# Performance work log

Hardware: AMD Instinct MI355X
Metric: run time of the kernel (lower is better)

Reference implementation:

```python
import jax, jax.numpy as jnp
import numpy as np

N, E, DIM, HEADS = 40000, 640000, 128, 8
HD = DIM // HEADS  # per-head dim
NEG_SLOPE = 0.2


def setup_inputs() -> dict:
    key = jax.random.key(0)
    ks = jax.random.split(key, 10)
    s = 1.0 / np.sqrt(DIM)
    return {
        "x": jax.random.normal(ks[0], (N, DIM), dtype=jnp.float32),
        "edge_index": jax.random.randint(ks[1], (2, E), 0, N, dtype=jnp.int64),
        "W_src": jax.random.normal(ks[2], (DIM, DIM), dtype=jnp.float32) * s,
        "b_src": jnp.zeros((DIM,), dtype=jnp.float32),
        "W_dst": jax.random.normal(ks[3], (DIM, DIM), dtype=jnp.float32) * s,
        "b_dst": jnp.zeros((DIM,), dtype=jnp.float32),
        "att": jax.random.normal(ks[4], (HEADS, HD), dtype=jnp.float32) * (1.0 / np.sqrt(HD)),
        "bias_out": jnp.zeros((DIM,), dtype=jnp.float32),
        "ln_gamma": jnp.ones((DIM,), dtype=jnp.float32),
        "ln_beta": jnp.zeros((DIM,), dtype=jnp.float32),
    }


def reference(x, edge_index, W_src, b_src, W_dst, b_dst, att, bias_out, ln_gamma, ln_beta):
    n = x.shape[0]
    # PyG GATv2Conv default: add self loops
    loops = jnp.arange(n, dtype=edge_index.dtype)
    src = jnp.concatenate([edge_index[0], loops])  # message source j
    dst = jnp.concatenate([edge_index[1], loops])  # message target i

    xs = (x @ W_src + b_src).reshape(n, HEADS, HD)  # [N,H,C]
    xd = (x @ W_dst + b_dst).reshape(n, HEADS, HD)

    # per-edge GATv2 attention logits
    e = xs[src] + xd[dst]                                   # [Et,H,C]
    e = jnp.where(e >= 0, e, NEG_SLOPE * e)                 # LeakyReLU(0.2)
    logits = jnp.einsum('ehc,hc->eh', e, att)               # [Et,H]

    # segment softmax over incoming edges of each dst node
    m = jax.ops.segment_max(logits, dst, num_segments=n)    # [N,H]
    ex = jnp.exp(logits - m[dst])
    denom = jax.ops.segment_sum(ex, dst, num_segments=n)    # [N,H]
    alpha = ex / denom[dst]                                  # [Et,H]

    # weighted scatter-add of source features
    msg = xs[src] * alpha[:, :, None]                       # [Et,H,C]
    out = jax.ops.segment_sum(msg, dst, num_segments=n)     # [N,H,C]
    out = out.reshape(n, DIM) + bias_out

    # dropout is identity in eval mode; residual + LayerNorm + GELU
    h = out + x
    mu = jnp.mean(h, axis=-1, keepdims=True)
    var = jnp.var(h, axis=-1, keepdims=True)
    h = (h - mu) / jnp.sqrt(var + 1e-5) * ln_gamma + ln_beta
    return jax.nn.gelu(h, approximate=False)
```

## Files before the change

kernel.cpp:

```cpp
#include <hip/hip_runtime.h>

typedef unsigned int uint;
typedef unsigned short ushort;
typedef __attribute__((ext_vector_type(8))) short short8;
typedef __attribute__((ext_vector_type(4))) float f32x4;

__device__ __forceinline__ float b2f(ushort u) {
    return __uint_as_float(((uint)u) << 16);
}
__device__ __forceinline__ ushort f2b(float f) {
    uint u = __float_as_uint(f);
    u += 0x7FFFu + ((u >> 16) & 1u);
    return (ushort)(u >> 16);
}
__device__ __forceinline__ float fast_exp2(float v) {
    float r;
    asm volatile("v_exp_f32 %0, %1" : "=v"(r) : "v"(v));
    return r;
}

template<int CTRL>
__device__ __forceinline__ float dpp_add(float v) {
    int s = __float_as_int(v);
    int d = __builtin_amdgcn_update_dpp(s, s, CTRL, 0xF, 0xF, true);
    return v + __int_as_float(d);
}

#define LDW 136

__global__ __launch_bounds__(512) void gemm_kernel(
    const float* __restrict__ x,
    const float* __restrict__ Wsrc, const float* __restrict__ bsrc,
    const float* __restrict__ Wdst, const float* __restrict__ bdst,
    ushort* __restrict__ xs, float* __restrict__ xd,
    int n, int* __restrict__ deg)
{
    __shared__ ushort WtS[128 * LDW];
    __shared__ ushort WtD[128 * LDW];
    int t = threadIdx.x;
    int gid = blockIdx.x * 512 + t;
    if (gid < n) deg[gid] = 1;
    for (int i = t * 4; i < 128 * 128; i += 512 * 4) {
        int k = i >> 7, c = i & 127;
        float4 wS = *(const float4*)(Wsrc + i);
        float4 wD = *(const float4*)(Wdst + i);
        WtS[(c + 0) * LDW + k] = f2b(wS.x);
        WtS[(c + 1) * LDW + k] = f2b(wS.y);
        WtS[(c + 2) * LDW + k] = f2b(wS.z);
        WtS[(c + 3) * LDW + k] = f2b(wS.w);
        WtD[(c + 0) * LDW + k] = f2b(wD.x);
        WtD[(c + 1) * LDW + k] = f2b(wD.y);
        WtD[(c + 2) * LDW + k] = f2b(wD.z);
        WtD[(c + 3) * LDW + k] = f2b(wD.w);
    }
    __syncthreads();

    int wave = t >> 6, lane = t & 63;
    int r = lane & 15, q = lane >> 4;
    int row = blockIdx.x * 128 + wave * 16 + r;
    f32x4 accS[8], accD[8];
#pragma unroll
    for (int i = 0; i < 8; i++) { accS[i] = (f32x4)(0.f); accD[i] = (f32x4)(0.f); }

#pragma unroll
    for (int kk = 0; kk < 4; kk++) {
        float v[8];
#pragma unroll
        for (int j = 0; j < 8; j++) v[j] = 0.f;
        if (row < n) {
            const float4* src = (const float4*)(x + (size_t)row * 128 + kk * 32 + q * 8);
            float4 p0 = src[0], p1 = src[1];
            v[0] = p0.x; v[1] = p0.y; v[2] = p0.z; v[3] = p0.w;
            v[4] = p1.x; v[5] = p1.y; v[6] = p1.z; v[7] = p1.w;
        }
        short8 ah, al;
#pragma unroll
        for (int j = 0; j < 8; j++) {
            ushort h = f2b(v[j]);
            ah[j] = (short)h;
            al[j] = (short)f2b(v[j] - b2f(h));
        }
#pragma unroll
        for (int ct = 0; ct < 8; ct++) {
            int off = (ct * 16 + r) * LDW + kk * 32 + q * 8;
            short8 bS = *(const short8*)(WtS + off);
            short8 bD = *(const short8*)(WtD + off);
            accS[ct] = __builtin_amdgcn_mfma_f32_16x16x32_bf16(ah, bS, accS[ct], 0, 0, 0);
            accS[ct] = __builtin_amdgcn_mfma_f32_16x16x32_bf16(al, bS, accS[ct], 0, 0, 0);
            accD[ct] = __builtin_amdgcn_mfma_f32_16x16x32_bf16(ah, bD, accD[ct], 0, 0, 0);
            accD[ct] = __builtin_amdgcn_mfma_f32_16x16x32_bf16(al, bD, accD[ct], 0, 0, 0);
        }
    }
    int rbase = blockIdx.x * 128 + wave * 16 + q * 4;
#pragma unroll
    for (int ct = 0; ct < 8; ct++) {
        int col = ct * 16 + r;
        float bS = bsrc[col];
        float bD = bdst[col];
#pragma unroll
        for (int rg = 0; rg < 4; rg++) {
            int orow = rbase + rg;
            if (orow < n) {
                xs[(size_t)orow * 128 + col] = f2b(accS[ct][rg] + bS);
                xd[(size_t)orow * 128 + col] = accD[ct][rg] + bD;
            }
        }
    }
}

__global__ void count_kernel(const int* __restrict__ ei, int E,
                             int* __restrict__ deg) {
    __shared__ int f_s;
    if (threadIdx.x < 64) {
        int w = ei[2 * threadIdx.x + 1];
        unsigned long long nz = __ballot(w != 0);
        if (threadIdx.x == 0) f_s = (nz == 0ULL) ? 1 : 0;
    }
    __syncthreads();
    int f = f_s;
    int e = blockIdx.x * 256 + threadIdx.x;
    if (e < E) {
        int d = f ? ei[2 * E + 2 * e] : ei[E + e];
        atomicAdd(&deg[d], 1);
    }
}

__global__ __launch_bounds__(1024) void scan_blk(
    const int* __restrict__ deg, int* __restrict__ lpre,
    int* __restrict__ bsum, int n)
{
    __shared__ int ws[16];
    __shared__ int wp[16];
    int t = threadIdx.x, lane = t & 63, w = t >> 6;
    int g = blockIdx.x * 1024 + t;
    int v = (g < n) ? deg[g] : 0;
    int inc = v;
#pragma unroll
    for (int off = 1; off < 64; off <<= 1) {
        int sh = __shfl_up(inc, off);
        if (lane >= off) inc += sh;
    }
    if (lane == 63) ws[w] = inc;
    __syncthreads();
    if (t == 0) {
        int run = 0;
#pragma unroll
        for (int i = 0; i < 16; i++) { wp[i] = run; run += ws[i]; }
        bsum[blockIdx.x] = run;
    }
    __syncthreads();
    if (g < n) lpre[g] = wp[w] + inc - v;
}

__global__ __launch_bounds__(1024) void scan_fix(
    const int* __restrict__ lpre, const int* __restrict__ bsum,
    const int* __restrict__ deg, int* __restrict__ row_start,
    int* __restrict__ cursor, int n)
{
    __shared__ int boff_s;
    int t = threadIdx.x, b = blockIdx.x;
    if (t < 64) {
        int v = 0;
        for (int i = t; i < b; i += 64) v += bsum[i];
#pragma unroll
        for (int off = 32; off >= 1; off >>= 1) v += __shfl_xor(v, off);
        if (t == 0) boff_s = v;
    }
    __syncthreads();
    int g = b * 1024 + t;
    if (g < n) {
        int rs = lpre[g] + boff_s;
        row_start[g] = rs;
        cursor[g] = rs;
        if (g == n - 1) row_start[n] = rs + deg[g];
    }
}

__global__ void fill_kernel(const int* __restrict__ ei, int E, int n,
                            int* __restrict__ cursor, int* __restrict__ esrc) {
    __shared__ int f_s;
    if (threadIdx.x < 64) {
        int w = ei[2 * threadIdx.x + 1];
        unsigned long long nz = __ballot(w != 0);
        if (threadIdx.x == 0) f_s = (nz == 0ULL) ? 1 : 0;
    }
    __syncthreads();
    int f = f_s;
    int idx = blockIdx.x * 256 + threadIdx.x;
    if (idx < E) {
        int s = f ? ei[2 * idx]         : ei[idx];
        int d = f ? ei[2 * E + 2 * idx] : ei[E + idx];
        int pos = atomicAdd(&cursor[d], 1);
        esrc[pos] = s;
    } else if (idx < E + n) {
        int i = idx - E;
        int pos = atomicAdd(&cursor[i], 1);
        esrc[pos] = i;
    }
}

__global__ __launch_bounds__(64) void node_kernel(
    const ushort* __restrict__ xs, const float* __restrict__ xd,
    const float* __restrict__ x,  const float* __restrict__ att,
    const float* __restrict__ bias_out, const float* __restrict__ gamma,
    const float* __restrict__ beta,
    const int* __restrict__ row_start, const int* __restrict__ esrc,
    float* __restrict__ out, int n)
{
    int lane = threadIdx.x;
    int node = blockIdx.x;
    if (node >= n) return;
    int q = lane >> 4, r = lane & 15;
    int cb = r * 8;

    const float LOG2E = 1.44269504088896f;
    const float A = 0.6f * LOG2E, B = 0.4f * LOG2E;

    float xdc[8], atc[8];
    {
        const float4* xp = (const float4*)(xd + (size_t)node * 128 + cb);
        float4 p0 = xp[0], p1 = xp[1];
        xdc[0]=p0.x; xdc[1]=p0.y; xdc[2]=p0.z; xdc[3]=p0.w;
        xdc[4]=p1.x; xdc[5]=p1.y; xdc[6]=p1.z; xdc[7]=p1.w;
        const float4* ap = (const float4*)(att + cb);
        float4 a0 = ap[0], a1 = ap[1];
        atc[0]=a0.x; atc[1]=a0.y; atc[2]=a0.z; atc[3]=a0.w;
        atc[4]=a1.x; atc[5]=a1.y; atc[6]=a1.z; atc[7]=a1.w;
    }
    float KL = 0.f;
#pragma unroll
    for (int i = 0; i < 8; i++) KL = fmaf(atc[i], xdc[i], KL);
    KL *= A;

    int start = row_start[node], end = row_start[node + 1];
    int end1 = end - 1;
    float s = 0.f, acc[8];
#pragma unroll
    for (int i = 0; i < 8; i++) acc[i] = 0.f;

    uint cboff = (uint)(cb);
    int j0 = esrc[min(start + q, end1)];
    uint4 raw = *(const uint4*)(xs + (uint)j0 * 128u + cboff);

    for (int base = start; base < end; base += 4) {
        int jn = esrc[min(base + 4 + q, end1)];
        uint4 rawn = *(const uint4*)(xs + (uint)jn * 128u + cboff);

        float v[8];
        v[0] = __uint_as_float(raw.x << 16); v[1] = __uint_as_float(raw.x & 0xFFFF0000u);
        v[2] = __uint_as_float(raw.y << 16); v[3] = __uint_as_float(raw.y & 0xFFFF0000u);
        v[4] = __uint_as_float(raw.z << 16); v[5] = __uint_as_float(raw.z & 0xFFFF0000u);
        v[6] = __uint_as_float(raw.w << 16); v[7] = __uint_as_float(raw.w & 0xFFFF0000u);

        float dv = 0.f, da = 0.f;
#pragma unroll
        for (int i = 0; i < 8; i++) {
            dv = fmaf(atc[i], v[i], dv);
            da = fmaf(atc[i], fabsf(v[i] + xdc[i]), da);
        }
        float P = fmaf(A, dv, fmaf(B, da, KL));
        P = dpp_add<0xB1>(P);
        float p = fast_exp2(P);
        p = (base + q < end) ? p : 0.f;
        s += p;
#pragma unroll
        for (int i = 0; i < 8; i++) acc[i] = fmaf(p, v[i], acc[i]);

        raw = rawn;
    }

#pragma unroll
    for (int off = 16; off <= 32; off <<= 1) {
        s += __shfl_xor(s, off);
#pragma unroll
        for (int i = 0; i < 8; i++) acc[i] += __shfl_xor(acc[i], off);
    }

    float inv = 1.f / s;
    float o[8];
    {
        const float4* bp = (const float4*)(bias_out + cb);
        const float4* xp = (const float4*)(x + (size_t)node * 128 + cb);
        float4 b0 = bp[0], b1 = bp[1], x0 = xp[0], x1 = xp[1];
        o[0] = fmaf(acc[0], inv, b0.x + x0.x); o[1] = fmaf(acc[1], inv, b0.y + x0.y);
        o[2] = fmaf(acc[2], inv, b0.z + x0.z); o[3] = fmaf(acc[3], inv, b0.w + x0.w);
        o[4] = fmaf(acc[4], inv, b1.x + x1.x); o[5] = fmaf(acc[5], inv, b1.y + x1.y);
        o[6] = fmaf(acc[6], inv, b1.z + x1.z); o[7] = fmaf(acc[7], inv, b1.w + x1.w);
    }
    float ssum = 0.f, ssq = 0.f;
#pragma unroll
    for (int i = 0; i < 8; i++) {
        ssum += o[i];
        ssq  = fmaf(o[i], o[i], ssq);
    }
#pragma unroll
    for (int off = 1; off <= 8; off <<= 1) {
        ssum += __shfl_xor(ssum, off);
        ssq  += __shfl_xor(ssq, off);
    }
    float mean = ssum * (1.f / 128.f);
    float var  = ssq  * (1.f / 128.f) - mean * mean;
    float rstd = rsqrtf(var + 1e-5f);

    if (q == 0) {
        const float4* gp = (const float4*)(gamma + cb);
        const float4* ep = (const float4*)(beta + cb);
        float4 g0 = gp[0], g1 = gp[1], e0 = ep[0], e1 = ep[1];
        float gch[8] = {g0.x, g0.y, g0.z, g0.w, g1.x, g1.y, g1.z, g1.w};
        float ech[8] = {e0.x, e0.y, e0.z, e0.w, e1.x, e1.y, e1.z, e1.w};
        float res[8];
#pragma unroll
        for (int i = 0; i < 8; i++) {
            float g = (o[i] - mean) * rstd * gch[i] + ech[i];
            res[i] = 0.5f * g * (1.f + erff(g * 0.70710678118654752f));
        }
        float4* op = (float4*)(out + (size_t)node * 128 + cb);
        float4 r0, r1;
        r0.x = res[0]; r0.y = res[1]; r0.z = res[2]; r0.w = res[3];
        r1.x = res[4]; r1.y = res[5]; r1.z = res[6]; r1.w = res[7];
        op[0] = r0; op[1] = r1;
    }
}

extern "C" void kernel_launch(void* const* d_in, const int* in_sizes, int n_in,
                              void* d_out, int out_size, void* d_ws, size_t ws_size,
                              hipStream_t stream)
{
    const float* x    = (const float*)d_in[0];
    const int*   ei   = (const int*)d_in[1];
    const float* Wsrc = (const float*)d_in[2];
    const float* bsrc = (const float*)d_in[3];
    const float* Wdst = (const float*)d_in[4];
    const float* bdst = (const float*)d_in[5];
    const float* att  = (const float*)d_in[6];
    const float* bout = (const float*)d_in[7];
    const float* gam  = (const float*)d_in[8];
    const float* bet  = (const float*)d_in[9];
    float* out = (float*)d_out;

    int n = in_sizes[0] / 128;
    int E = in_sizes[1] / 2;

    char* p = (char*)d_ws;
    auto alloc = [&](size_t bytes) {
        char* q = p;
        p += (bytes + 255) & ~((size_t)255);
        return q;
    };
    ushort* xs        = (ushort*)alloc((size_t)n * 128 * 2);
    float*  xd        = (float*)alloc((size_t)n * 128 * 4);
    int*    deg       = (int*)alloc((size_t)n * 4);
    int*    row_start = (int*)alloc((size_t)(n + 1) * 4);
    int*    cursor    = (int*)alloc((size_t)n * 4);
    int*    esrc      = (int*)alloc((size_t)(E + n) * 4);
    int     nblk      = (n + 1023) / 1024;
    int*    lpre      = (int*)alloc((size_t)nblk * 1024 * 4);
    int*    bsum      = (int*)alloc((size_t)nblk * 4);

    hipLaunchKernelGGL(gemm_kernel, dim3((n + 127) / 128), dim3(512), 0, stream,
                       x, Wsrc, bsrc, Wdst, bdst, xs, xd, n, deg);
    hipLaunchKernelGGL(count_kernel, dim3((E + 255) / 256), dim3(256), 0, stream,
                       ei, E, deg);
    hipLaunchKernelGGL(scan_blk, dim3(nblk), dim3(1024), 0, stream,
                       deg, lpre, bsum, n);
    hipLaunchKernelGGL(scan_fix, dim3(nblk), dim3(1024), 0, stream,
                       lpre, bsum, deg, row_start, cursor, n);
    hipLaunchKernelGGL(fill_kernel, dim3((E + n + 255) / 256), dim3(256), 0, stream,
                       ei, E, n, cursor, esrc);
    hipLaunchKernelGGL(node_kernel, dim3(n), dim3(64), 0, stream,
                       xs, xd, x, att, bout, gam, bet, row_start, esrc, out, n);
}
```

Before: 221.4 us.

## Fuse CSR build into one persistent kernel with software grid barriers

Replaces the count, two-pass scan and fill kernels with a single 128-block persistent kernel that uses atomic-counter grid barriers between phases, and reads edge indices with vectorized uint4 loads. Degree init moves to a memset. The node kernel drops the min() clamp on esrc by padding esrc with 64 zeros, and gets a launch_bounds occupancy hint. This removes several kernel launches and their inter-kernel gaps, but the fused kernel runs on only 128 blocks, which may underuse the device for the atomic scatter phases. The spin barriers also rely on every block being resident at once.

```diff
diff --git a/kernel.cpp b/kernel.cpp
--- a/kernel.cpp
+++ b/kernel.cpp
@@ -32,14 +32,11 @@
     const float* __restrict__ x,
     const float* __restrict__ Wsrc, const float* __restrict__ bsrc,
     const float* __restrict__ Wdst, const float* __restrict__ bdst,
-    ushort* __restrict__ xs, float* __restrict__ xd,
-    int n, int* __restrict__ deg)
+    ushort* __restrict__ xs, float* __restrict__ xd, int n)
 {
     __shared__ ushort WtS[128 * LDW];
     __shared__ ushort WtD[128 * LDW];
     int t = threadIdx.x;
-    int gid = blockIdx.x * 512 + t;
-    if (gid < n) deg[gid] = 1;
     for (int i = t * 4; i < 128 * 128; i += 512 * 4) {
         int k = i >> 7, c = i & 127;
         float4 wS = *(const float4*)(Wsrc + i);
@@ -108,33 +105,62 @@
     }
 }
 
-__global__ void count_kernel(const int* __restrict__ ei, int E,
-                             int* __restrict__ deg) {
+#define CSRB 128
+#define CSRT 256
+
+__device__ __forceinline__ void gbar(int* ctr, int target) {
+    __syncthreads();
+    if (threadIdx.x == 0) {
+        __threadfence();
+        atomicAdd(ctr, 1);
+        while (atomicAdd(ctr, 0) < target) {}
+        __threadfence();
+    }
+    __syncthreads();
+}
+
+__global__ __launch_bounds__(CSRT) void csr_kernel(
+    const int* __restrict__ ei, int E, int n,
+    int* __restrict__ deg, int* __restrict__ row_start,
+    int* __restrict__ cursor, int* __restrict__ esrc,
+    int* __restrict__ bsum, int* __restrict__ bpre, int* __restrict__ bar)
+{
+    int t = threadIdx.x, b = blockIdx.x;
+    int lane = t & 63, w = t >> 6;
     __shared__ int f_s;
-    if (threadIdx.x < 64) {
-        int w = ei[2 * threadIdx.x + 1];
-        unsigned long long nz = __ballot(w != 0);
-        if (threadIdx.x == 0) f_s = (nz == 0ULL) ? 1 : 0;
+    __shared__ int ws[4], wp[4];
+    if (t < 64) {
+        int wv = ei[2 * t + 1];
+        unsigned long long nz = __ballot(wv != 0);
+        if (t == 0) f_s = (nz == 0ULL) ? 1 : 0;
     }
     __syncthreads();
     int f = f_s;
-    int e = blockIdx.x * 256 + threadIdx.x;
-    if (e < E) {
-        int d = f ? ei[2 * E + 2 * e] : ei[E + e];
-        atomicAdd(&deg[d], 1);
-    }
-}
-
-__global__ __launch_bounds__(1024) void scan_blk(
-    const int* __restrict__ deg, int* __restrict__ lpre,
-    int* __restrict__ bsum, int n)
-{
-    __shared__ int ws[16];
-    __shared__ int wp[16];
-    int t = threadIdx.x, lane = t & 63, w = t >> 6;
-    int g = blockIdx.x * 1024 + t;
-    int v = (g < n) ? deg[g] : 0;
-    int inc = v;
+    const int NT = CSRB * CSRT;
+    int g = b * CSRT + t;
+
+    if (f) {
+        int half = E >> 1;
+        const uint4* dp = ((const uint4*)ei) + (E >> 1);
+        for (int i = g; i < half; i += NT) {
+            uint4 dq = dp[i];
+            atomicAdd(&deg[(int)dq.x], 1);
+            atomicAdd(&deg[(int)dq.z], 1);
+        }
+        if ((E & 1) && g == 0) atomicAdd(&deg[ei[2 * E + 2 * (E - 1)]], 1);
+    } else {
+        for (int e = g; e < E; e += NT) atomicAdd(&deg[ei[E + e]], 1);
+    }
+    gbar(&bar[0], CSRB);
+
+    const int C = (n + CSRB - 1) / CSRB;
+    int lo = b * C;
+    int hi = min(lo + C, n);
+    int i0 = lo + 2 * t, i1 = i0 + 1;
+    int d0 = (i0 < hi) ? deg[i0] + 1 : 0;
+    int d1 = (i1 < hi) ? deg[i1] + 1 : 0;
+    int s2 = d0 + d1;
+    int inc = s2;
 #pragma unroll
     for (int off = 1; off < 64; off <<= 1) {
         int sh = __shfl_up(inc, off);
@@ -145,61 +171,68 @@
     if (t == 0) {
         int run = 0;
 #pragma unroll
-        for (int i = 0; i < 16; i++) { wp[i] = run; run += ws[i]; }
-        bsum[blockIdx.x] = run;
-    }
-    __syncthreads();
-    if (g < n) lpre[g] = wp[w] + inc - v;
-}
-
-__global__ __launch_bounds__(1024) void scan_fix(
-    const int* __restrict__ lpre, const int* __restrict__ bsum,
-    const int* __restrict__ deg, int* __restrict__ row_start,
-    int* __restrict__ cursor, int n)
-{
-    __shared__ int boff_s;
-    int t = threadIdx.x, b = blockIdx.x;
-    if (t < 64) {
-        int v = 0;
-        for (int i = t; i < b; i += 64) v += bsum[i];
-#pragma unroll
-        for (int off = 32; off >= 1; off >>= 1) v += __shfl_xor(v, off);
-        if (t == 0) boff_s = v;
-    }
-    __syncthreads();
-    int g = b * 1024 + t;
-    if (g < n) {
-        int rs = lpre[g] + boff_s;
-        row_start[g] = rs;
-        cursor[g] = rs;
-        if (g == n - 1) row_start[n] = rs + deg[g];
-    }
-}
-
-__global__ void fill_kernel(const int* __restrict__ ei, int E, int n,
-                            int* __restrict__ cursor, int* __restrict__ esrc) {
-    __shared__ int f_s;
-    if (threadIdx.x < 64) {
-        int w = ei[2 * threadIdx.x + 1];
-        unsigned long long nz = __ballot(w != 0);
-        if (threadIdx.x == 0) f_s = (nz == 0ULL) ? 1 : 0;
-    }
-    __syncthreads();
-    int f = f_s;
-    int idx = blockIdx.x * 256 + threadIdx.x;
-    if (idx < E) {
-        int s = f ? ei[2 * idx]         : ei[idx];
-        int d = f ? ei[2 * E + 2 * idx] : ei[E + idx];
-        int pos = atomicAdd(&cursor[d], 1);
-        esrc[pos] = s;
-    } else if (idx < E + n) {
-        int i = idx - E;
-        int pos = atomicAdd(&cursor[i], 1);
-        esrc[pos] = i;
-    }
-}
-
-__global__ __launch_bounds__(64) void node_kernel(
+        for (int i = 0; i < 4; i++) { wp[i] = run; run += ws[i]; }
+        atomicExch(&bsum[b], run);
+    }
+    __syncthreads();
+    int excl = wp[w] + inc - s2;
+    gbar(&bar[1], CSRB);
+
+    if (b == 0) {
+        int v = (t < CSRB) ? atomicAdd(&bsum[t], 0) : 0;
+        int inc2 = v;
+#pragma unroll
+        for (int off = 1; off < 64; off <<= 1) {
+            int sh = __shfl_up(inc2, off);
+            if (lane >= off) inc2 += sh;
+        }
+        if (lane == 63) ws[w] = inc2;
+        __syncthreads();
+        if (t == 0) {
+            int run = 0;
+#pragma unroll
+            for (int i = 0; i < 4; i++) { wp[i] = run; run += ws[i]; }
+            row_start[n] = run;
+        }
+        __syncthreads();
+        int ex2 = wp[w] + inc2 - v;
+        if (t < CSRB) atomicExch(&bpre[t], ex2);
+    }
+    gbar(&bar[2], CSRB);
+
+    int boff = atomicAdd(&bpre[b], 0);
+    if (i0 < hi) { int rs = boff + excl;      row_start[i0] = rs; atomicExch(&cursor[i0], rs); }
+    if (i1 < hi) { int rs = boff + excl + d0; row_start[i1] = rs; atomicExch(&cursor[i1], rs); }
+    gbar(&bar[3], CSRB);
+
+    if (f) {
+        int half = E >> 1;
+        const uint4* sp = (const uint4*)ei;
+        const uint4* dp = sp + (E >> 1);
+        for (int i = g; i < half; i += NT) {
+            uint4 sq = sp[i], dq = dp[i];
+            int p0 = atomicAdd(&cursor[(int)dq.x], 1); esrc[p0] = (int)sq.x;
+            int p1 = atomicAdd(&cursor[(int)dq.z], 1); esrc[p1] = (int)sq.z;
+        }
+        if ((E & 1) && g == 0) {
+            int e = E - 1;
+            int p0 = atomicAdd(&cursor[ei[2 * E + 2 * e]], 1);
+            esrc[p0] = ei[2 * e];
+        }
+    } else {
+        for (int e = g; e < E; e += NT) {
+            int p0 = atomicAdd(&cursor[ei[E + e]], 1);
+            esrc[p0] = ei[e];
+        }
+    }
+    for (int i = g; i < n; i += NT) {
+        int p0 = atomicAdd(&cursor[i], 1);
+        esrc[p0] = i;
+    }
+    if (g < 64) esrc[E + n + g] = 0;
+}
+
+__global__ __launch_bounds__(64, 4) void node_kernel(
     const ushort* __restrict__ xs, const float* __restrict__ xd,
     const float* __restrict__ x,  const float* __restrict__ att,
     const float* __restrict__ bias_out, const float* __restrict__ gamma,
@@ -233,17 +266,16 @@
     KL *= A;
 
     int start = row_start[node], end = row_start[node + 1];
-    int end1 = end - 1;
     float s = 0.f, acc[8];
 #pragma unroll
     for (int i = 0; i < 8; i++) acc[i] = 0.f;
 
-    uint cboff = (uint)(cb);
-    int j0 = esrc[min(start + q, end1)];
+    uint cboff = (uint)cb;
+    int j0 = esrc[start + q];
     uint4 raw = *(const uint4*)(xs + (uint)j0 * 128u + cboff);
 
     for (int base = start; base < end; base += 4) {
-        int jn = esrc[min(base + 4 + q, end1)];
+        int jn = esrc[base + 4 + q];
         uint4 rawn = *(const uint4*)(xs + (uint)jn * 128u + cboff);
 
         float v[8];
@@ -311,8 +343,8 @@
         float res[8];
 #pragma unroll
         for (int i = 0; i < 8; i++) {
-            float g = (o[i] - mean) * rstd * gch[i] + ech[i];
-            res[i] = 0.5f * g * (1.f + erff(g * 0.70710678118654752f));
+            float gg = (o[i] - mean) * rstd * gch[i] + ech[i];
+            res[i] = 0.5f * gg * (1.f + erff(gg * 0.70710678118654752f));
         }
         float4* op = (float4*)(out + (size_t)node * 128 + cb);
         float4 r0, r1;
@@ -349,24 +381,19 @@
     };
     ushort* xs        = (ushort*)alloc((size_t)n * 128 * 2);
     float*  xd        = (float*)alloc((size_t)n * 128 * 4);
-    int*    deg       = (int*)alloc((size_t)n * 4);
+    int*    deg       = (int*)alloc((size_t)(n + 4) * 4);
+    int*    bar       = deg + n;
     int*    row_start = (int*)alloc((size_t)(n + 1) * 4);
     int*    cursor    = (int*)alloc((size_t)n * 4);
-    int*    esrc      = (int*)alloc((size_t)(E + n) * 4);
-    int     nblk      = (n + 1023) / 1024;
-    int*    lpre      = (int*)alloc((size_t)nblk * 1024 * 4);
-    int*    bsum      = (int*)alloc((size_t)nblk * 4);
-
+    int*    esrc      = (int*)alloc((size_t)(E + n + 64) * 4);
+    int*    bsum      = (int*)alloc((size_t)CSRB * 4);
+    int*    bpre      = (int*)alloc((size_t)CSRB * 4);
+
+    hipMemsetAsync(deg, 0, (size_t)(n + 4) * 4, stream);
     hipLaunchKernelGGL(gemm_kernel, dim3((n + 127) / 128), dim3(512), 0, stream,
-                       x, Wsrc, bsrc, Wdst, bdst, xs, xd, n, deg);
-    hipLaunchKernelGGL(count_kernel, dim3((E + 255) / 256), dim3(256), 0, stream,
-                       ei, E, deg);
-    hipLaunchKernelGGL(scan_blk, dim3(nblk), dim3(1024), 0, stream,
-                       deg, lpre, bsum, n);
-    hipLaunchKernelGGL(scan_fix, dim3(nblk), dim3(1024), 0, stream,
-                       lpre, bsum, deg, row_start, cursor, n);
-    hipLaunchKernelGGL(fill_kernel, dim3((E + n + 255) / 256), dim3(256), 0, stream,
-                       ei, E, n, cursor, esrc);
+                       x, Wsrc, bsrc, Wdst, bdst, xs, xd, n);
+    hipLaunchKernelGGL(csr_kernel, dim3(CSRB), dim3(CSRT), 0, stream,
+                       ei, E, n, deg, row_start, cursor, esrc, bsum, bpre, bar);
     hipLaunchKernelGGL(node_kernel, dim3(n), dim3(64), 0, stream,
                        xs, xd, x, att, bout, gam, bet, row_start, esrc, out, n);
 }
```

After: 250.8 us. 13.3% more time.
